# Kernel optimization log

Measured on AMD Instinct MI355X. Metric: run time of the kernel, lower is better.

## Reference

```python
import jax, jax.numpy as jnp
import numpy as np

D_MODEL = 1024
NUM_HEADS = 16
D_K = D_MODEL // NUM_HEADS
THETA = 10000.0


def _rope(x, pos):
    # x: [H, B, S, D_K]; pos: [S] int. Interleaved-pair rotation (matrix-form RoPE).
    d2 = D_K // 2
    inv_freq = THETA ** (-(2.0 * jnp.arange(d2, dtype=jnp.float32)) / D_K)  # [d2]
    ang = pos.astype(jnp.float32)[:, None] * inv_freq[None, :]              # [S, d2]
    sin, cos = jnp.sin(ang), jnp.cos(ang)
    xr = x.reshape(*x.shape[:-1], d2, 2)
    x0, x1 = xr[..., 0], xr[..., 1]
    out0 = cos * x0 - sin * x1
    out1 = sin * x0 + cos * x1
    return jnp.stack([out0, out1], axis=-1).reshape(x.shape)


def setup_inputs() -> dict:
    key = jax.random.key(0)
    ks = jax.random.split(key, 5)
    scale = 1.0 / np.sqrt(D_MODEL)
    return {
        "x": jax.random.normal(ks[0], (4, 2048, D_MODEL), dtype=jnp.float32),
        "token_positions": jnp.arange(2048, dtype=jnp.int32),
        "Wq": jax.random.normal(ks[1], (D_MODEL, D_MODEL), dtype=jnp.float32) * scale,
        "Wk": jax.random.normal(ks[2], (D_MODEL, D_MODEL), dtype=jnp.float32) * scale,
        "Wv": jax.random.normal(ks[3], (D_MODEL, D_MODEL), dtype=jnp.float32) * scale,
        "Wo": jax.random.normal(ks[4], (D_MODEL, D_MODEL), dtype=jnp.float32) * scale,
    }


def reference(x, token_positions, Wq, Wk, Wv, Wo):
    B, S, D = x.shape
    H, dk = NUM_HEADS, D_K
    # Projections (Linear stores weight [out,in], applies x @ W.T)
    def proj(W):
        return (x @ W.T).reshape(B, S, H, dk).transpose(2, 0, 1, 3)  # [H,B,S,dk]
    q, k, v = proj(Wq), proj(Wk), proj(Wv)
    q = _rope(q, token_positions)
    k = _rope(k, token_positions)
    scores = jnp.einsum("hbsd,hbtd->hbst", q, k) / jnp.sqrt(jnp.float32(dk))
    causal = jnp.tril(jnp.ones((S, S), dtype=bool))
    scores = jnp.where(causal, scores, jnp.float32(-1e9))
    attn = jax.nn.softmax(scores, axis=-1)
    out = jnp.einsum("hbst,hbtd->hbsd", attn, v)       # [H,B,S,dk]
    out = out.transpose(1, 2, 0, 3).reshape(B, S, D)   # [B,S,D]
    return out @ Wo.T
```

## Files before the change

### kernel.cpp

```cpp
#include <hip/hip_runtime.h>

typedef __bf16 bf16;
typedef bf16 bf16x8 __attribute__((ext_vector_type(8)));
typedef bf16 bf16x4 __attribute__((ext_vector_type(4)));
typedef float floatx4 __attribute__((ext_vector_type(4)));

#define D_MODEL 1024
#define SEQ     2048
#define NB      4
#define NH      16
#define DKH     64
#define ROPE_L2 0.4152410118609203f

__device__ __forceinline__ floatx4 mfma16(bf16x8 a, bf16x8 b, floatx4 c) {
  return __builtin_amdgcn_mfma_f32_16x16x32_bf16(a, b, c, 0, 0, 0);
}

__device__ __forceinline__ void gload_lds16(void* lds_uniform, const void* gsrc) {
  __builtin_amdgcn_global_load_lds(
      (__attribute__((address_space(1))) unsigned int*)(void*)(gsrc),
      (__attribute__((address_space(3))) unsigned int*)lds_uniform,
      16, 0, 0);
}

__global__ __launch_bounds__(256) void cvt_all(
    const float4* __restrict__ x,
    const float4* __restrict__ wq, const float4* __restrict__ wk,
    const float4* __restrict__ wv, const float4* __restrict__ wo,
    bf16x4* __restrict__ xb,
    bf16x4* __restrict__ b0, bf16x4* __restrict__ b1,
    bf16x4* __restrict__ b2, bf16x4* __restrict__ b3) {
  const int i = blockIdx.x * 256 + threadIdx.x;
  const float4* src;
  bf16x4* dst;
  int off;
  if (i < (1 << 21)) {
    src = x; dst = xb; off = i;
  } else {
    const int j = i - (1 << 21);
    const int widx = j >> 18;
    off = j & ((1 << 18) - 1);
    src = (widx == 0) ? wq : (widx == 1) ? wk : (widx == 2) ? wv : wo;
    dst = (widx == 0) ? b0 : (widx == 1) ? b1 : (widx == 2) ? b2 : b3;
  }
  const float4 v = src[off];
  bf16x4 o;
  o[0] = (bf16)v.x; o[1] = (bf16)v.y; o[2] = (bf16)v.z; o[3] = (bf16)v.w;
  dst[off] = o;
}

__global__ __launch_bounds__(256) void rope_table(const int* __restrict__ tokpos,
                                                  float2* __restrict__ tab) {
  const int i = blockIdx.x * 256 + threadIdx.x;
  const int s = i >> 5, i2 = i & 31;
  const float ang = (float)tokpos[s] * exp2f(-(float)i2 * ROPE_L2);
  float sn, cs;
  sincosf(ang, &sn, &cs);
  tab[i] = make_float2(sn, cs);
}

#define QK_SRC_DECL(Aptr, Bq, Bk)                                              \
  const int c_0 = w * 64 + lane;                                               \
  const int row0_ = c_0 >> 2, seg0_ = (c_0 & 3) ^ ((row0_ >> 1) & 3);          \
  const int c_1 = c_0 + 256;                                                   \
  const int row1_ = c_1 >> 2, seg1_ = (c_1 & 3) ^ ((row1_ >> 1) & 3);          \
  const bf16* asrc0 = (Aptr) + (size_t)(bm + row0_) * D_MODEL + seg0_ * 8;     \
  const bf16* asrc1 = (Aptr) + (size_t)(bm + row1_) * D_MODEL + seg1_ * 8;     \
  const bf16* bqsrc0 = (Bq) + (size_t)(bn + row0_) * D_MODEL + seg0_ * 8;      \
  const bf16* bqsrc1 = (Bq) + (size_t)(bn + row1_) * D_MODEL + seg1_ * 8;      \
  const bf16* bksrc0 = (Bk) + (size_t)(bn + row0_) * D_MODEL + seg0_ * 8;      \
  const bf16* bksrc1 = (Bk) + (size_t)(bn + row1_) * D_MODEL + seg1_ * 8;     \
  const int gsw = (g ^ ((r >> 1) & 3)) * 8;

#define QKA(buf) ((char*)LDSBUF + (buf) * 8192)
#define QKQ(buf) ((char*)LDSBUF + 16384 + (buf) * 8192)
#define QKK(buf) ((char*)LDSBUF + 32768 + (buf) * 8192)

#define QK_STAGE(buf, kk)                                                      \
  gload_lds16(QKA(buf) + (w * 64) * 16, asrc0 + (kk));                         \
  gload_lds16(QKQ(buf) + (w * 64) * 16, bqsrc0 + (kk));                        \
  gload_lds16(QKK(buf) + (w * 64) * 16, bksrc0 + (kk));                        \
  gload_lds16(QKA(buf) + (w * 64 + 256) * 16, asrc1 + (kk));                   \
  gload_lds16(QKQ(buf) + (w * 64 + 256) * 16, bqsrc1 + (kk));                  \
  gload_lds16(QKK(buf) + (w * 64 + 256) * 16, bksrc1 + (kk));

#define ROPEW(mm, nn, CV, SC)                                                  \
  _Pragma("unroll")                                                            \
  for (int reg = 0; reg < 4; ++reg) {                                          \
    const int srow = mm * 16 + g * 4 + reg;                                    \
    const int c = wc * 64 + nn * 16 + r;                                       \
    const int s_ = (bm + wr * 64 + srow) & (SEQ - 1);                          \
    const int d_ = c & 63;                                                     \
    float v = CV[reg];                                                         \
    float pp = __shfl_xor(v, 1);                                               \
    const float2 sc2 = ropetab[s_ * 32 + (d_ >> 1)];                           \
    float res = ((d_ & 1) == 0) ? (sc2.y * v - sc2.x * pp)                     \
                                : (sc2.x * pp + sc2.y * v);                    \
    res *= SC;                                                                 \
    *(bf16*)((char*)LDSBUF + srow * 272 + c * 2) = (bf16)res;                  \
  }

#define QK_EPI(A00,A01,A02,A03,A10,A11,A12,A13,A20,A21,A22,A23,A30,A31,A32,A33,\
               dst0, SC)                                                       \
  _Pragma("unroll")                                                            \
  for (int p = 0; p < 2; ++p) {                                                \
    if (wr == p) {                                                             \
      ROPEW(0, 0, A00, SC) ROPEW(0, 1, A01, SC) ROPEW(0, 2, A02, SC)           \
      ROPEW(0, 3, A03, SC) ROPEW(1, 0, A10, SC) ROPEW(1, 1, A11, SC)           \
      ROPEW(1, 2, A12, SC) ROPEW(1, 3, A13, SC) ROPEW(2, 0, A20, SC)           \
      ROPEW(2, 1, A21, SC) ROPEW(2, 2, A22, SC) ROPEW(2, 3, A23, SC)           \
      ROPEW(3, 0, A30, SC) ROPEW(3, 1, A31, SC) ROPEW(3, 2, A32, SC)           \
      ROPEW(3, 3, A33, SC)                                                     \
    }                                                                          \
    __syncthreads();                                                           \
    const int s_r = tid >> 2, quad = tid & 3;                                  \
    const int grow = bm + p * 64 + s_r;                                        \
    const int b_ = grow >> 11, s_ = grow & (SEQ - 1);                          \
    const int h_ = hbase + (quad >> 1);                                        \
    bf16* dstp = (dst0) + ((size_t)(b_ * NH + h_) * SEQ + s_) * DKH +          \
                 (quad & 1) * 32;                                              \
    _Pragma("unroll")                                                          \
    for (int j = 0; j < 4; ++j)                                                \
      *(float4*)(dstp + j * 8) =                                               \
          *(const float4*)((char*)LDSBUF + s_r * 272 + quad * 64 + j * 16);    \
    __syncthreads();                                                           \
  }

__global__ __launch_bounds__(256, 2) void gemm_qk(
    const bf16* __restrict__ A,
    const bf16* __restrict__ Wq, const bf16* __restrict__ Wk,
    bf16* __restrict__ Qd, bf16* __restrict__ Kd,
    const float2* __restrict__ ropetab) {
  __shared__ __align__(16) char LDSBUF[49152];
  const int orig = (int)(blockIdx.x + (blockIdx.y << 3));
  const int l = (orig & 7) * 64 + (orig >> 3);
  const int bm = (l >> 3) * 128, bn = (l & 7) * 128;
  const int tid = threadIdx.x, lane = tid & 63, w = tid >> 6;
  const int wr = w >> 1, wc = w & 1;
  const int r = lane & 15, g = lane >> 4;

  floatx4 q00 = {}, q01 = {}, q02 = {}, q03 = {};
  floatx4 q10 = {}, q11 = {}, q12 = {}, q13 = {};
  floatx4 q20 = {}, q21 = {}, q22 = {}, q23 = {};
  floatx4 q30 = {}, q31 = {}, q32 = {}, q33 = {};
  floatx4 k00 = {}, k01 = {}, k02 = {}, k03 = {};
  floatx4 k10 = {}, k11 = {}, k12 = {}, k13 = {};
  floatx4 k20 = {}, k21 = {}, k22 = {}, k23 = {};
  floatx4 k30 = {}, k31 = {}, k32 = {}, k33 = {};

  QK_SRC_DECL(A, Wq, Wk)
  QK_STAGE(0, 0)
  __syncthreads();
  int cub = 0;
  for (int kt = 0; kt < 32; ++kt) {
    if (kt + 1 < 32) { QK_STAGE(cub ^ 1, (kt + 1) * 32) }
    const bf16* Abase = (const bf16*)QKA(cub) + (wr * 64 + r) * 32 + gsw;
    const bf16* Qbase = (const bf16*)QKQ(cub) + (wc * 64 + r) * 32 + gsw;
    const bf16* Kbase = (const bf16*)QKK(cub) + (wc * 64 + r) * 32 + gsw;
    bf16x8 a0 = *(const bf16x8*)(Abase + 0 * 512);
    bf16x8 a1 = *(const bf16x8*)(Abase + 1 * 512);
    bf16x8 a2 = *(const bf16x8*)(Abase + 2 * 512);
    bf16x8 a3 = *(const bf16x8*)(Abase + 3 * 512);
    bf16x8 bq0 = *(const bf16x8*)(Qbase + 0 * 512);
    bf16x8 bq1 = *(const bf16x8*)(Qbase + 1 * 512);
    bf16x8 bq2 = *(const bf16x8*)(Qbase + 2 * 512);
    bf16x8 bq3 = *(const bf16x8*)(Qbase + 3 * 512);
    bf16x8 bk0 = *(const bf16x8*)(Kbase + 0 * 512);
    bf16x8 bk1 = *(const bf16x8*)(Kbase + 1 * 512);
    bf16x8 bk2 = *(const bf16x8*)(Kbase + 2 * 512);
    bf16x8 bk3 = *(const bf16x8*)(Kbase + 3 * 512);
    __builtin_amdgcn_s_setprio(1);
    q00 = mfma16(a0, bq0, q00); q01 = mfma16(a0, bq1, q01);
    q02 = mfma16(a0, bq2, q02); q03 = mfma16(a0, bq3, q03);
    k00 = mfma16(a0, bk0, k00); k01 = mfma16(a0, bk1, k01);
    k02 = mfma16(a0, bk2, k02); k03 = mfma16(a0, bk3, k03);
    q10 = mfma16(a1, bq0, q10); q11 = mfma16(a1, bq1, q11);
    q12 = mfma16(a1, bq2, q12); q13 = mfma16(a1, bq3, q13);
    k10 = mfma16(a1, bk0, k10); k11 = mfma16(a1, bk1, k11);
    k12 = mfma16(a1, bk2, k12); k13 = mfma16(a1, bk3, k13);
    q20 = mfma16(a2, bq0, q20); q21 = mfma16(a2, bq1, q21);
    q22 = mfma16(a2, bq2, q22); q23 = mfma16(a2, bq3, q23);
    k20 = mfma16(a2, bk0, k20); k21 = mfma16(a2, bk1, k21);
    k22 = mfma16(a2, bk2, k22); k23 = mfma16(a2, bk3, k23);
    q30 = mfma16(a3, bq0, q30); q31 = mfma16(a3, bq1, q31);
    q32 = mfma16(a3, bq2, q32); q33 = mfma16(a3, bq3, q33);
    k30 = mfma16(a3, bk0, k30); k31 = mfma16(a3, bk1, k31);
    k32 = mfma16(a3, bk2, k32); k33 = mfma16(a3, bk3, k33);
    __builtin_amdgcn_s_setprio(0);
    __syncthreads();
    cub ^= 1;
  }

  const int hbase = bn >> 6;
  QK_EPI(q00,q01,q02,q03,q10,q11,q12,q13,q20,q21,q22,q23,q30,q31,q32,q33,
         Qd, 0.125f)
  QK_EPI(k00,k01,k02,k03,k10,k11,k12,k13,k20,k21,k22,k23,k30,k31,k32,k33,
         Kd, 1.0f)
}

#define GEMM_ACC_DECL                              \
  floatx4 c00 = {}, c01 = {}, c02 = {}, c03 = {};  \
  floatx4 c10 = {}, c11 = {}, c12 = {}, c13 = {};  \
  floatx4 c20 = {}, c21 = {}, c22 = {}, c23 = {};  \
  floatx4 c30 = {}, c31 = {}, c32 = {}, c33 = {};

#define AS_BASE(buf) ((char*)LDSBUF + (buf) * 8192)
#define BS_BASE(buf) ((char*)LDSBUF + 16384 + (buf) * 8192)

#define GEMM_STAGE(buf, kk)                                                    \
  gload_lds16(AS_BASE(buf) + (w * 64) * 16, asrc0 + (kk));                     \
  gload_lds16(BS_BASE(buf) + (w * 64) * 16, bsrc0 + (kk));                     \
  gload_lds16(AS_BASE(buf) + (w * 64 + 256) * 16, asrc1 + (kk));               \
  gload_lds16(BS_BASE(buf) + (w * 64 + 256) * 16, bsrc1 + (kk));

#define GEMM_MAINLOOP(Aptr, Bptr)                                              \
  const int c_0 = w * 64 + lane;                                               \
  const int row0_ = c_0 >> 2, seg0_ = (c_0 & 3) ^ ((row0_ >> 1) & 3);          \
  const int c_1 = c_0 + 256;                                                   \
  const int row1_ = c_1 >> 2, seg1_ = (c_1 & 3) ^ ((row1_ >> 1) & 3);          \
  const bf16* asrc0 = (Aptr) + (size_t)(bm + row0_) * D_MODEL + seg0_ * 8;     \
  const bf16* asrc1 = (Aptr) + (size_t)(bm + row1_) * D_MODEL + seg1_ * 8;     \
  const bf16* bsrc0 = (Bptr) + (size_t)(bn + row0_) * D_MODEL + seg0_ * 8;     \
  const bf16* bsrc1 = (Bptr) + (size_t)(bn + row1_) * D_MODEL + seg1_ * 8;     \
  const int gsw = (g ^ ((r >> 1) & 3)) * 8;                                    \
  GEMM_STAGE(0, 0)                                                             \
  __syncthreads();                                                             \
  int cub = 0;                                                                 \
  for (int kt = 0; kt < 32; ++kt) {                                            \
    if (kt + 1 < 32) { GEMM_STAGE(cub ^ 1, (kt + 1) * 32) }                    \
    const bf16* Abase = (const bf16*)AS_BASE(cub) + (wr * 64 + r) * 32 + gsw;  \
    const bf16* Bbase = (const bf16*)BS_BASE(cub) + (wc * 64 + r) * 32 + gsw;  \
    bf16x8 a0 = *(const bf16x8*)(Abase + 0 * 512);                             \
    bf16x8 a1 = *(const bf16x8*)(Abase + 1 * 512);                             \
    bf16x8 a2 = *(const bf16x8*)(Abase + 2 * 512);                             \
    bf16x8 a3 = *(const bf16x8*)(Abase + 3 * 512);                             \
    bf16x8 b0 = *(const bf16x8*)(Bbase + 0 * 512);                             \
    bf16x8 b1 = *(const bf16x8*)(Bbase + 1 * 512);                             \
    bf16x8 b2 = *(const bf16x8*)(Bbase + 2 * 512);                             \
    bf16x8 b3 = *(const bf16x8*)(Bbase + 3 * 512);                             \
    __builtin_amdgcn_s_setprio(1);                                             \
    c00 = mfma16(a0, b0, c00); c01 = mfma16(a0, b1, c01);                      \
    c02 = mfma16(a0, b2, c02); c03 = mfma16(a0, b3, c03);                      \
    c10 = mfma16(a1, b0, c10); c11 = mfma16(a1, b1, c11);                      \
    c12 = mfma16(a1, b2, c12); c13 = mfma16(a1, b3, c13);                      \
    c20 = mfma16(a2, b0, c20); c21 = mfma16(a2, b1, c21);                      \
    c22 = mfma16(a2, b2, c22); c23 = mfma16(a2, b3, c23);                      \
    c30 = mfma16(a3, b0, c30); c31 = mfma16(a3, b1, c31);                      \
    c32 = mfma16(a3, b2, c32); c33 = mfma16(a3, b3, c33);                      \
    __builtin_amdgcn_s_setprio(0);                                             \
    __syncthreads();                                                           \
    cub ^= 1;                                                                  \
  }

#define V_WRITE(mm, nn, CV)                                                    \
  _Pragma("unroll")                                                            \
  for (int reg = 0; reg < 4; ++reg) {                                          \
    const int crow = nn * 16 + r;                                              \
    const int s_l = wr * 64 + mm * 16 + g * 4 + reg;                           \
    *(bf16*)((char*)LDSBUF + crow * 272 + s_l * 2) = (bf16)CV[reg];            \
  }

__global__ __launch_bounds__(256, 3) void gemm_v(const bf16* __restrict__ A,
                                                 const bf16* __restrict__ Wv,
                                                 bf16* __restrict__ Vd) {
  __shared__ __align__(16) char LDSBUF[32768];
  const int orig = (int)(blockIdx.x + (blockIdx.y << 3));
  const int l = (orig & 7) * 64 + (orig >> 3);
  const int bm = (l >> 3) * 128, bn = (l & 7) * 128;
  const int tid = threadIdx.x, lane = tid & 63, w = tid >> 6;
  const int wr = w >> 1, wc = w & 1;
  const int r = lane & 15, g = lane >> 4;
  GEMM_ACC_DECL
  GEMM_MAINLOOP(A, Wv)

  const int hbase = bn >> 6;
  const int b_ = bm >> 11, sbase = bm & (SEQ - 1);
#pragma unroll
  for (int p = 0; p < 2; ++p) {
    if (wc == p) {
      V_WRITE(0, 0, c00) V_WRITE(0, 1, c01) V_WRITE(0, 2, c02) V_WRITE(0, 3, c03)
      V_WRITE(1, 0, c10) V_WRITE(1, 1, c11) V_WRITE(1, 2, c12) V_WRITE(1, 3, c13)
      V_WRITE(2, 0, c20) V_WRITE(2, 1, c21) V_WRITE(2, 2, c22) V_WRITE(2, 3, c23)
      V_WRITE(3, 0, c30) V_WRITE(3, 1, c31) V_WRITE(3, 2, c32) V_WRITE(3, 3, c33)
    }
    __syncthreads();
    const int c_r = tid >> 2, quad = tid & 3;
    const int c = p * 64 + c_r;
    const int h_ = hbase + (c >> 6), d_ = c & 63;
    bf16* dstp = Vd + ((size_t)(b_ * NH + h_) * DKH + d_) * SEQ + sbase + quad * 32;
#pragma unroll
    for (int j = 0; j < 4; ++j)
      *(float4*)(dstp + j * 8) =
          *(const float4*)((char*)LDSBUF + c_r * 272 + quad * 64 + j * 16);
    __syncthreads();
  }
}

#define OUT_EPI(mm, nn, CV)                                                    \
  _Pragma("unroll")                                                            \
  for (int reg = 0; reg < 4; ++reg) {                                          \
    const int grow = bm + wr * 64 + mm * 16 + g * 4 + reg;                     \
    const int gcol = bn + wc * 64 + nn * 16 + r;                               \
    C[(size_t)grow * D_MODEL + gcol] = CV[reg];                                \
  }

__global__ __launch_bounds__(256, 3) void gemm_out(const bf16* __restrict__ A,
                                                   const bf16* __restrict__ Bw,
                                                   float* __restrict__ C) {
  __shared__ __align__(16) char LDSBUF[32768];
  const int orig = (int)(blockIdx.x + (blockIdx.y << 3));
  const int l = (orig & 7) * 64 + (orig >> 3);
  const int bm = (l >> 3) * 128, bn = (l & 7) * 128;
  const int tid = threadIdx.x, lane = tid & 63, w = tid >> 6;
  const int wr = w >> 1, wc = w & 1;
  const int r = lane & 15, g = lane >> 4;
  GEMM_ACC_DECL
  GEMM_MAINLOOP(A, Bw)
  OUT_EPI(0, 0, c00) OUT_EPI(0, 1, c01) OUT_EPI(0, 2, c02) OUT_EPI(0, 3, c03)
  OUT_EPI(1, 0, c10) OUT_EPI(1, 1, c11) OUT_EPI(1, 2, c12) OUT_EPI(1, 3, c13)
  OUT_EPI(2, 0, c20) OUT_EPI(2, 1, c21) OUT_EPI(2, 2, c22) OUT_EPI(2, 3, c23)
  OUT_EPI(3, 0, c30) OUT_EPI(3, 1, c31) OUT_EPI(3, 2, c32) OUT_EPI(3, 3, c33)
}

__global__ __launch_bounds__(256, 3) void attn128(const bf16* __restrict__ Q,
                                                  const bf16* __restrict__ Kk,
                                                  const bf16* __restrict__ Vt,
                                                  bf16* __restrict__ AO) {
  const int orig = (int)(blockIdx.x + (blockIdx.y << 4));
  const int i_ = orig >> 3;
  const int qt = 15 - (i_ >> 3);
  const int bh = (orig & 7) * 8 + (i_ & 7);
  const int b = bh >> 4, h = bh & 15;
  const int tid = threadIdx.x, lane = tid & 63, w = tid >> 6;
  const int r = lane & 15, g = lane >> 4;
  const int q0 = qt * 128 + w * 32;

  const bf16* Qb = Q + (size_t)bh * SEQ * DKH;
  const bf16* Kb = Kk + (size_t)bh * SEQ * DKH;
  const bf16* Vb = Vt + (size_t)bh * DKH * SEQ;

  __shared__ bf16 Ks[2][64 * 64];
  __shared__ bf16 Vs[2][64 * 64];
  __shared__ bf16 Ps[4][32 * 64];

  int ldsoff[2];
  const char* ksrc[2];
  const char* vsrc[2];
#pragma unroll
  for (int j = 0; j < 2; ++j) {
    const int L = (w * 64 + lane + 256 * j) * 16;
    const int S = L ^ (((L >> 7) & 7) << 4);
    ldsoff[j] = (w * 64 + 256 * j) * 16;
    ksrc[j] = (const char*)Kb + S;
    vsrc[j] = (const char*)Vb + (size_t)(S >> 7) * (SEQ * 2) + (S & 127);
  }

#define ATTN_STAGE(buf, tt)                                                   \
  _Pragma("unroll")                                                           \
  for (int j = 0; j < 2; ++j) {                                               \
    gload_lds16((char*)Ks[buf] + ldsoff[j], ksrc[j] + (size_t)(tt) * 8192);   \
    gload_lds16((char*)Vs[buf] + ldsoff[j], vsrc[j] + (size_t)(tt) * 128);    \
  }

#define SM_TILE(MASKED)                                                        \
  _Pragma("unroll")                                                            \
  for (int m = 0; m < 2; ++m) {                                                \
    const int qq_ = q0 + m * 16 + r;                                           \
    const int wl_ = m * 16 + r;                                                \
    _Pragma("unroll")                                                          \
    for (int nf = 0; nf < 4; ++nf) {                                           \
      floatx4 p;                                                               \
      _Pragma("unroll")                                                        \
      for (int reg = 0; reg < 4; ++reg) {                                      \
        float pe = exp2f(fmaf(sc[m][nf][reg], 1.442695041f, -17.31234049f));   \
        if (MASKED && (t0 + nf * 16 + g * 4 + reg > qq_)) pe = 0.f;            \
        p[reg] = pe;                                                           \
      }                                                                        \
      l2[m] += p;                                                              \
      unsigned u0, u1;                                                         \
      asm("v_cvt_pk_bf16_f32 %0, %1, %2" : "=v"(u0) : "v"(p[0]), "v"(p[1]));   \
      asm("v_cvt_pk_bf16_f32 %0, %1, %2" : "=v"(u1) : "v"(p[2]), "v"(p[3]));   \
      const int pb = (wl_ * 128 + nf * 32 + g * 8) ^ ((wl_ & 7) << 4);         \
      *(uint2*)((char*)Ps[w] + pb) = make_uint2(u0, u1);                       \
    }                                                                          \
  }

  bf16x8 qf[2][2];
#pragma unroll
  for (int m = 0; m < 2; ++m)
#pragma unroll
    for (int ks = 0; ks < 2; ++ks)
      qf[m][ks] = *(const bf16x8*)(Qb + (size_t)(q0 + m * 16 + r) * DKH + ks * 32 + g * 8);

  floatx4 o[2][4] = {};
  floatx4 l2[2] = {};

  const int nt = 2 * qt + 2;
  ATTN_STAGE(0, 0)
  __syncthreads();
  int cu = 0;
  for (int t = 0; t < nt; ++t) {
    if (t + 1 < nt) ATTN_STAGE(cu ^ 1, t + 1)
    const int t0 = t * 64;

    floatx4 sc[2][4];
    __builtin_amdgcn_s_setprio(1);
#pragma unroll
    for (int nf = 0; nf < 4; ++nf) {
      const int row = nf * 16 + r;
      const int off0 = (row * 128 + g * 16) ^ ((row & 7) << 4);
      bf16x8 kf0 = *(const bf16x8*)((const char*)Ks[cu] + off0);
      bf16x8 kf1 = *(const bf16x8*)((const char*)Ks[cu] + (off0 ^ 64));
      sc[0][nf] = mfma16(kf1, qf[0][1], mfma16(kf0, qf[0][0], floatx4{0.f, 0.f, 0.f, 0.f}));
      sc[1][nf] = mfma16(kf1, qf[1][1], mfma16(kf0, qf[1][0], floatx4{0.f, 0.f, 0.f, 0.f}));
    }
    __builtin_amdgcn_s_setprio(0);

    const bool edge = (t0 + 63 > q0);
    if (edge) {
      SM_TILE(1)
    } else {
      SM_TILE(0)
    }
    asm volatile("s_waitcnt lgkmcnt(0)" ::: "memory");

    bf16x8 pf[2][2];
#pragma unroll
    for (int m = 0; m < 2; ++m)
#pragma unroll
      for (int ks = 0; ks < 2; ++ks) {
        const int prow = m * 16 + r;
        const int ab = (prow * 128 + ks * 64 + g * 16) ^ ((prow & 7) << 4);
        pf[m][ks] = *(const bf16x8*)((const char*)Ps[w] + ab);
      }
    __builtin_amdgcn_s_setprio(1);
#pragma unroll
    for (int nf = 0; nf < 4; ++nf) {
      const int vrow = nf * 16 + r;
      const int vb0 = (vrow * 128 + g * 16) ^ ((vrow & 7) << 4);
      bf16x8 vf0 = *(const bf16x8*)((const char*)Vs[cu] + vb0);
      bf16x8 vf1 = *(const bf16x8*)((const char*)Vs[cu] + (vb0 ^ 64));
#pragma unroll
      for (int m = 0; m < 2; ++m)
        o[m][nf] = mfma16(pf[m][1], vf1, mfma16(pf[m][0], vf0, o[m][nf]));
    }
    __builtin_amdgcn_s_setprio(0);
    __syncthreads();
    cu ^= 1;
  }

  float lsm[2];
#pragma unroll
  for (int m = 0; m < 2; ++m) {
    float ls = l2[m][0] + l2[m][1] + l2[m][2] + l2[m][3];
    ls += __shfl_xor(ls, 16);
    ls += __shfl_xor(ls, 32);
    lsm[m] = ls;
  }
  float linv[2][4];
#pragma unroll
  for (int m = 0; m < 2; ++m)
#pragma unroll
    for (int reg = 0; reg < 4; ++reg)
      linv[m][reg] = 1.f / __shfl(lsm[m], g * 4 + reg);

#pragma unroll
  for (int m = 0; m < 2; ++m)
#pragma unroll
    for (int nf = 0; nf < 4; ++nf)
#pragma unroll
      for (int reg = 0; reg < 4; ++reg) {
        const int s = q0 + m * 16 + g * 4 + reg;
        const int d = nf * 16 + r;
        const float val = o[m][nf][reg] * linv[m][reg];
        AO[((size_t)(b * SEQ + s)) * D_MODEL + h * DKH + d] = (bf16)val;
      }
}

extern "C" void kernel_launch(void* const* d_in, const int* in_sizes, int n_in,
                              void* d_out, int out_size, void* d_ws, size_t ws_size,
                              hipStream_t stream) {
  const float* x = (const float*)d_in[0];
  const int* tokpos = (const int*)d_in[1];
  const float* Wq = (const float*)d_in[2];
  const float* Wk = (const float*)d_in[3];
  const float* Wv = (const float*)d_in[4];
  const float* Wo = (const float*)d_in[5];
  float* out = (float*)d_out;

  char* ws = (char*)d_ws;
  if (ws_size < (72ull << 20)) return;

  bf16* xb  = (bf16*)(ws);
  bf16* wb0 = (bf16*)(ws + (16ull << 20));
  bf16* wb1 = (bf16*)(ws + (18ull << 20));
  bf16* wb2 = (bf16*)(ws + (20ull << 20));
  bf16* wb3 = (bf16*)(ws + (22ull << 20));
  bf16* Qb  = (bf16*)(ws + (24ull << 20));
  bf16* Kb  = (bf16*)(ws + (40ull << 20));
  bf16* Vt  = (bf16*)(ws + (56ull << 20));
  bf16* AO  = (bf16*)(ws);
  float2* ropetab = (float2*)d_out;

  rope_table<<<256, 256, 0, stream>>>(tokpos, ropetab);
  cvt_all<<<12288, 256, 0, stream>>>((const float4*)x, (const float4*)Wq,
                                     (const float4*)Wk, (const float4*)Wv,
                                     (const float4*)Wo, (bf16x4*)xb,
                                     (bf16x4*)wb0, (bf16x4*)wb1,
                                     (bf16x4*)wb2, (bf16x4*)wb3);

  gemm_qk<<<dim3(8, 64), 256, 0, stream>>>(xb, wb0, wb1, Qb, Kb, ropetab);
  gemm_v<<<dim3(8, 64), 256, 0, stream>>>(xb, wb2, Vt);
  attn128<<<dim3(16, 64), 256, 0, stream>>>(Qb, Kb, Vt, AO);
  gemm_out<<<dim3(8, 64), 256, 0, stream>>>(AO, wb3, out);
}
```

Before: 178.6 us.

## Replace LDS P round-trip with ds_bpermute, raise occupancy, interleave causal tiles

Probabilities for the PV matmul are now kept in registers and reshuffled into the MFMA A-operand layout with ds_bpermute, instead of being written to a per-wave LDS buffer and read back. This removes the Ps shared array and its store/wait/load sequence, lowering LDS usage. Launch bounds rise to 4 blocks per CU, and the query-tile order alternates heavy and light causal tiles to balance work across blocks. The trade-off is 16 bpermute operations per tile plus selects, and tighter register limits at the higher occupancy target, which could cause spills.

```diff
diff --git a/kernel.cpp b/kernel.cpp
--- a/kernel.cpp
+++ b/kernel.cpp
@@ -4,6 +4,7 @@
 typedef bf16 bf16x8 __attribute__((ext_vector_type(8)));
 typedef bf16 bf16x4 __attribute__((ext_vector_type(4)));
 typedef float floatx4 __attribute__((ext_vector_type(4)));
+typedef int intx4 __attribute__((ext_vector_type(4)));
 
 #define D_MODEL 1024
 #define SEQ     2048
@@ -322,13 +323,14 @@
   OUT_EPI(3, 0, c30) OUT_EPI(3, 1, c31) OUT_EPI(3, 2, c32) OUT_EPI(3, 3, c33)
 }
 
-__global__ __launch_bounds__(256, 3) void attn128(const bf16* __restrict__ Q,
+__global__ __launch_bounds__(256, 4) void attn128(const bf16* __restrict__ Q,
                                                   const bf16* __restrict__ Kk,
                                                   const bf16* __restrict__ Vt,
                                                   bf16* __restrict__ AO) {
   const int orig = (int)(blockIdx.x + (blockIdx.y << 4));
   const int i_ = orig >> 3;
-  const int qt = 15 - (i_ >> 3);
+  const int vq = i_ >> 3;
+  const int qt = (vq & 1) ? (vq >> 1) : (15 - (vq >> 1));
   const int bh = (orig & 7) * 8 + (i_ & 7);
   const int b = bh >> 4, h = bh & 15;
   const int tid = threadIdx.x, lane = tid & 63, w = tid >> 6;
@@ -341,7 +343,10 @@
 
   __shared__ bf16 Ks[2][64 * 64];
   __shared__ bf16 Vs[2][64 * 64];
-  __shared__ bf16 Ps[4][32 * 64];
+
+  const int bpi0 = ((lane & 15) | ((((lane >> 4) << 1) & 3) << 4)) << 2;
+  const int bpi1 = ((lane & 15) | (((((lane >> 4) << 1) | 1) & 3) << 4)) << 2;
+  const bool ghi = (g >> 1) != 0;
 
   int ldsoff[2];
   const char* ksrc[2];
@@ -366,7 +371,6 @@
   _Pragma("unroll")                                                            \
   for (int m = 0; m < 2; ++m) {                                                \
     const int qq_ = q0 + m * 16 + r;                                           \
-    const int wl_ = m * 16 + r;                                                \
     _Pragma("unroll")                                                          \
     for (int nf = 0; nf < 4; ++nf) {                                           \
       floatx4 p;                                                               \
@@ -380,8 +384,8 @@
       unsigned u0, u1;                                                         \
       asm("v_cvt_pk_bf16_f32 %0, %1, %2" : "=v"(u0) : "v"(p[0]), "v"(p[1]));   \
       asm("v_cvt_pk_bf16_f32 %0, %1, %2" : "=v"(u1) : "v"(p[2]), "v"(p[3]));   \
-      const int pb = (wl_ * 128 + nf * 32 + g * 8) ^ ((wl_ & 7) << 4);         \
-      *(uint2*)((char*)Ps[w] + pb) = make_uint2(u0, u1);                       \
+      upk[m][nf][0] = (int)u0;                                                 \
+      upk[m][nf][1] = (int)u1;                                                 \
     }                                                                          \
   }
 
@@ -394,6 +398,7 @@
 
   floatx4 o[2][4] = {};
   floatx4 l2[2] = {};
+  int upk[2][4][2];
 
   const int nt = 2 * qt + 2;
   ATTN_STAGE(0, 0)
@@ -422,17 +427,28 @@
     } else {
       SM_TILE(0)
     }
-    asm volatile("s_waitcnt lgkmcnt(0)" ::: "memory");
 
     bf16x8 pf[2][2];
 #pragma unroll
     for (int m = 0; m < 2; ++m)
 #pragma unroll
       for (int ks = 0; ks < 2; ++ks) {
-        const int prow = m * 16 + r;
-        const int ab = (prow * 128 + ks * 64 + g * 16) ^ ((prow & 7) << 4);
-        pf[m][ks] = *(const bf16x8*)((const char*)Ps[w] + ab);
+        const int A0 = __builtin_amdgcn_ds_bpermute(bpi0, upk[m][2 * ks][0]);
+        const int A1 = __builtin_amdgcn_ds_bpermute(bpi0, upk[m][2 * ks][1]);
+        const int B0 = __builtin_amdgcn_ds_bpermute(bpi0, upk[m][2 * ks + 1][0]);
+        const int B1 = __builtin_amdgcn_ds_bpermute(bpi0, upk[m][2 * ks + 1][1]);
+        const int C0 = __builtin_amdgcn_ds_bpermute(bpi1, upk[m][2 * ks][0]);
+        const int C1 = __builtin_amdgcn_ds_bpermute(bpi1, upk[m][2 * ks][1]);
+        const int E0 = __builtin_amdgcn_ds_bpermute(bpi1, upk[m][2 * ks + 1][0]);
+        const int E1 = __builtin_amdgcn_ds_bpermute(bpi1, upk[m][2 * ks + 1][1]);
+        intx4 di;
+        di[0] = ghi ? B0 : A0;
+        di[1] = ghi ? B1 : A1;
+        di[2] = ghi ? E0 : C0;
+        di[3] = ghi ? E1 : C1;
+        pf[m][ks] = __builtin_bit_cast(bf16x8, di);
       }
+
     __builtin_amdgcn_s_setprio(1);
 #pragma unroll
     for (int nf = 0; nf < 4; ++nf) {
```

Result: slower. 212.2 us (+18.9%).
